# Optimization experiments

Measured on AMD Instinct MI355X. Metric: run time of the kernel, lower is better.

## Reference

```python
import jax, jax.numpy as jnp
import numpy as np

B, D, V = 2048, 512, 50304


def setup_inputs() -> dict:
    key = jax.random.key(0)
    ks = jax.random.split(key, 7)
    scale = 1.0 / np.sqrt(D)
    return {
        "student_h": jax.random.normal(ks[0], (B, D), dtype=jnp.float32) * scale,
        "student_c": jax.random.normal(ks[1], (V, D), dtype=jnp.float32) * scale,
        "teacher_h": jax.random.normal(ks[2], (B, D), dtype=jnp.float32) * scale,
        "teacher_c": jax.random.normal(ks[3], (V, D), dtype=jnp.float32) * scale,
        "ce_coeff": jax.random.uniform(ks[4], (B,), dtype=jnp.float32),
        "kl_coeff": jax.random.uniform(ks[5], (B,), dtype=jnp.float32),
        "targets": jax.random.randint(ks[6], (B,), 0, V, dtype=jnp.int64),
    }


def reference(student_h, student_c, teacher_h, teacher_c, ce_coeff, kl_coeff, targets):
    # Fused linear head: student/teacher logits over the full vocab  [B, V]
    s_logits = jnp.einsum("bd,vd->bv", student_h, student_c)
    t_logits = jnp.einsum("bd,vd->bv", teacher_h, teacher_c)

    s_lse = jax.nn.logsumexp(s_logits, axis=1)  # [B]
    t_lse = jax.nn.logsumexp(t_logits, axis=1)  # [B]

    # Cross-entropy per row: lse - logit[target]
    tgt_logit = jnp.take_along_axis(s_logits, targets[:, None], axis=1)[:, 0]
    ce = s_lse - tgt_logit  # [B]

    # KL(teacher || student) per row
    log_ps = s_logits - s_lse[:, None]
    log_pt = t_logits - t_lse[:, None]
    pt = jnp.exp(log_pt)
    kl = jnp.sum(pt * (log_pt - log_ps), axis=1)  # [B]

    # Per-row coefficients absorb any reduction weighting (as in the kernel)
    loss = jnp.sum(ce_coeff * ce + kl_coeff * kl)
    return loss
```

## Files before the change

kernel.cpp:

```cpp
#include <hip/hip_runtime.h>
#include <hip/hip_fp8.h>

#define B_ 2048
#define D_ 512
#define V_ 50304
#define NROWB 16
#define NCOLB 393
#define NWG (NROWB * NCOLB)
#define LOG2E 1.44269504088896340736f
#define LN2 0.69314718055994530942f

typedef __attribute__((ext_vector_type(4))) float f32x4;
typedef __attribute__((ext_vector_type(2))) unsigned long ulx2;
typedef unsigned char u8;

__device__ inline void gload16(const void* g, void* l) {
  __builtin_amdgcn_global_load_lds((const __attribute__((address_space(1))) void*)g,
                                   (__attribute__((address_space(3))) void*)l, 16, 0, 0);
}

__global__ void cast8_kernel(const float* __restrict__ src, uint2* __restrict__ dst,
                             float scale, int n8) {
  int i = blockIdx.x * blockDim.x + threadIdx.x;
  int stride = gridDim.x * blockDim.x;
  const float4* s4 = (const float4*)src;
  for (; i < n8; i += stride) {
    float4 a = s4[2 * i], b = s4[2 * i + 1];
    union { u8 c[8]; uint2 u; } p;
    p.c[0] = __hip_fp8_e4m3(a.x * scale).__x;
    p.c[1] = __hip_fp8_e4m3(a.y * scale).__x;
    p.c[2] = __hip_fp8_e4m3(a.z * scale).__x;
    p.c[3] = __hip_fp8_e4m3(a.w * scale).__x;
    p.c[4] = __hip_fp8_e4m3(b.x * scale).__x;
    p.c[5] = __hip_fp8_e4m3(b.y * scale).__x;
    p.c[6] = __hip_fp8_e4m3(b.z * scale).__x;
    p.c[7] = __hip_fp8_e4m3(b.w * scale).__x;
    dst[i] = p.u;
  }
}

__global__ void tgt_kernel(const float* __restrict__ sh, const float* __restrict__ sc,
                           const int* __restrict__ targets, float* __restrict__ tgt_out) {
  int gid = blockIdx.x * blockDim.x + threadIdx.x;
  int w = gid >> 6, lane = gid & 63;
  if (w >= B_) return;
  int tgt = targets[w];
  const float4* a = (const float4*)(sh + (size_t)w * D_);
  const float4* b = (const float4*)(sc + (size_t)tgt * D_);
  float acc = 0.f;
#pragma unroll
  for (int i = 0; i < 2; ++i) {
    float4 x = a[lane + i * 64], y = b[lane + i * 64];
    acc += x.x * y.x + x.y * y.y + x.z * y.z + x.w * y.w;
  }
#pragma unroll
  for (int off = 1; off < 64; off <<= 1) acc += __shfl_xor(acc, off);
  if (lane == 0) tgt_out[w] = acc;
}

__global__ __launch_bounds__(256, 2) void lce_main(
    const u8* __restrict__ SH8, const u8* __restrict__ TH8,
    const u8* __restrict__ SC8, const u8* __restrict__ TC8,
    float* __restrict__ stats) {
  __shared__ __align__(16) u8 smem[2][2][128][128];

  const int tid = threadIdx.x;
  const int lane = tid & 63, w = tid >> 6;
  const int mat = w & 1;
  const int wr = w >> 1;
  const int rA = lane & 15;
  const int kg = lane >> 4;
  const int r7 = rA & 7;

  int hw = blockIdx.x;
  int lid = (hw & 7) * 786 + (hw >> 3);
  const int row0 = (lid & 15) * 128;
  const int col0 = (lid >> 4) * 128;

  const int srow_lo = (lane >> 3);
  const int sq = ((lane & 7) ^ srow_lo) * 16;
  const u8* gB[2] = {SC8 + (size_t)(col0 + w * 32 + srow_lo) * D_ + sq,
                     TC8 + (size_t)(col0 + w * 32 + srow_lo) * D_ + sq};

  const u8* gA = (mat ? TH8 : SH8) + (size_t)(row0 + wr * 64 + rA) * D_ + kg * 16;

  f32x4 acc[4][8];
#pragma unroll
  for (int i = 0; i < 4; ++i)
#pragma unroll
    for (int j = 0; j < 8; ++j) acc[i][j] = (f32x4){0.f, 0.f, 0.f, 0.f};

  ulx2 afr[2][2][4];

#define STAGE(buf, kk)                                                        \
  {                                                                           \
    _Pragma("unroll") for (int t = 0; t < 2; ++t) {                           \
      _Pragma("unroll") for (int i = 0; i < 4; ++i) {                         \
        gload16(gB[t] + (size_t)(i * 8) * D_ + (kk) * 128,                    \
                &smem[buf][t][w * 32 + i * 8][0]);                            \
      }                                                                       \
    }                                                                         \
  }

#define LOADA(par, kk)                                                        \
  {                                                                           \
    _Pragma("unroll") for (int mi = 0; mi < 4; ++mi) {                        \
      const u8* p = gA + (size_t)(mi * 16) * D_ + (kk) * 128;                 \
      afr[par][0][mi] = *(const ulx2*)p;                                      \
      afr[par][1][mi] = *(const ulx2*)(p + 64);                               \
    }                                                                         \
  }

  STAGE(0, 0);
  LOADA(0, 0);

#pragma unroll
  for (int kk = 0; kk < 4; ++kk) {
    const int par = kk & 1;
    if (kk < 3) {
      STAGE(par ^ 1, kk + 1);
      LOADA(par ^ 1, kk + 1);
    }
    if (kk < 3)
      asm volatile("s_waitcnt vmcnt(16)\n\ts_barrier" ::: "memory");
    else
      asm volatile("s_waitcnt vmcnt(8)\n\ts_barrier" ::: "memory");

#pragma unroll
    for (int hp = 0; hp < 2; ++hp) {
      ulx2 bfr[8];
#pragma unroll
      for (int ni = 0; ni < 8; ++ni)
        bfr[ni] = *(const ulx2*)&smem[par][mat][ni * 16 + rA][((hp * 4 + kg) ^ r7) * 16];
      __builtin_amdgcn_s_setprio(1);
#pragma unroll
      for (int mi = 0; mi < 4; ++mi)
#pragma unroll
        for (int ni = 0; ni < 8; ++ni) {
          acc[mi][ni] = __builtin_amdgcn_mfma_f32_16x16x32_fp8_fp8(
              (long)afr[par][hp][mi].x, (long)bfr[ni].x, acc[mi][ni], 0, 0, 0);
          acc[mi][ni] = __builtin_amdgcn_mfma_f32_16x16x32_fp8_fp8(
              (long)afr[par][hp][mi].y, (long)bfr[ni].y, acc[mi][ni], 0, 0, 0);
        }
      __builtin_amdgcn_s_setprio(0);
    }
    asm volatile("s_barrier" ::: "memory");
  }

  const float inv = 1.0f / 256.0f;
  float2* exch = (float2*)smem;

  if (mat == 0) {
#pragma unroll
    for (int mi = 0; mi < 4; ++mi)
#pragma unroll
      for (int ni = 0; ni < 8; ++ni)
#pragma unroll
        for (int rp = 0; rp < 2; ++rp) {
          float2 v = make_float2(acc[mi][ni][2 * rp] * inv, acc[mi][ni][2 * rp + 1] * inv);
          exch[(size_t)((((wr * 4 + mi) * 8 + ni) * 2 + rp) * 64 + lane)] = v;
        }
  }
  asm volatile("s_waitcnt lgkmcnt(0)\n\ts_barrier" ::: "memory");

  if (mat == 0) {
#pragma unroll
    for (int mi = 0; mi < 4; ++mi) {
      float ssr[4] = {0.f, 0.f, 0.f, 0.f};
#pragma unroll
      for (int ni = 0; ni < 8; ++ni)
#pragma unroll
        for (int reg = 0; reg < 4; ++reg)
          ssr[reg] += __builtin_amdgcn_exp2f(acc[mi][ni][reg] * inv);
#pragma unroll
      for (int reg = 0; reg < 4; ++reg) {
        float v = ssr[reg];
#pragma unroll
        for (int off = 1; off < 16; off <<= 1) v += __shfl_xor(v, off);
        if (rA == 0)
          atomicAdd(&stats[(size_t)(row0 + wr * 64 + mi * 16 + kg * 4 + reg) * 3 + 0], v);
      }
    }
  } else {
#pragma unroll
    for (int mi = 0; mi < 4; ++mi) {
      float str[4] = {0.f, 0.f, 0.f, 0.f};
      float atr[4] = {0.f, 0.f, 0.f, 0.f};
#pragma unroll
      for (int ni = 0; ni < 8; ++ni)
#pragma unroll
        for (int rp = 0; rp < 2; ++rp) {
          float2 sv = exch[(size_t)((((wr * 4 + mi) * 8 + ni) * 2 + rp) * 64 + lane)];
          float tv0 = acc[mi][ni][2 * rp] * inv;
          float tv1 = acc[mi][ni][2 * rp + 1] * inv;
          float et0 = __builtin_amdgcn_exp2f(tv0);
          float et1 = __builtin_amdgcn_exp2f(tv1);
          str[2 * rp] += et0;
          str[2 * rp + 1] += et1;
          atr[2 * rp] += et0 * (tv0 - sv.x);
          atr[2 * rp + 1] += et1 * (tv1 - sv.y);
        }
#pragma unroll
      for (int reg = 0; reg < 4; ++reg) {
        float v = str[reg], u = atr[reg];
#pragma unroll
        for (int off = 1; off < 16; off <<= 1) {
          v += __shfl_xor(v, off);
          u += __shfl_xor(u, off);
        }
        if (rA == 0) {
          size_t r = (size_t)(row0 + wr * 64 + mi * 16 + kg * 4 + reg) * 3;
          atomicAdd(&stats[r + 1], v);
          atomicAdd(&stats[r + 2], u);
        }
      }
    }
  }
}

__global__ void finalize(const float* __restrict__ stats, const float* __restrict__ tgt,
                         const float* __restrict__ cec, const float* __restrict__ klc,
                         float* __restrict__ out) {
  __shared__ float red[16];
  int tid = threadIdx.x;
  float acc = 0.f;
  for (int r = tid; r < B_; r += 1024) {
    float ss = stats[r * 3 + 0], st = stats[r * 3 + 1], at = stats[r * 3 + 2];
    float s_lse = LN2 * __builtin_amdgcn_logf(ss);
    float t_lse = LN2 * __builtin_amdgcn_logf(st);
    float kl = s_lse - t_lse + LN2 * at / st;
    float ce = s_lse - tgt[r];
    acc += cec[r] * ce + klc[r] * kl;
  }
#pragma unroll
  for (int off = 1; off < 64; off <<= 1) acc += __shfl_xor(acc, off);
  if ((tid & 63) == 0) red[tid >> 6] = acc;
  __syncthreads();
  if (tid == 0) {
    float s = 0.f;
#pragma unroll
    for (int i = 0; i < 16; ++i) s += red[i];
    out[0] = s;
  }
}

extern "C" void kernel_launch(void* const* d_in, const int* in_sizes, int n_in,
                              void* d_out, int out_size, void* d_ws, size_t ws_size,
                              hipStream_t stream) {
  const float* sh = (const float*)d_in[0];
  const float* sc = (const float*)d_in[1];
  const float* th = (const float*)d_in[2];
  const float* tc = (const float*)d_in[3];
  const float* cec = (const float*)d_in[4];
  const float* klc = (const float*)d_in[5];
  const int* targets = (const int*)d_in[6];
  float* out = (float*)d_out;

  char* ws = (char*)d_ws;
  u8* SC8 = (u8*)ws;
  u8* TC8 = SC8 + (size_t)V_ * D_;
  u8* SH8 = TC8 + (size_t)V_ * D_;
  u8* TH8 = SH8 + (size_t)B_ * D_;
  float* stats = (float*)(TH8 + (size_t)B_ * D_);
  float* tgt = stats + (size_t)B_ * 3;

  hipMemsetAsync(stats, 0, (size_t)B_ * 3 * sizeof(float), stream);
  const float hscale = 16.0f * LOG2E;
  const float cscale = 16.0f;
  cast8_kernel<<<2048, 256, 0, stream>>>(sc, (uint2*)SC8, cscale, V_ * D_ / 8);
  cast8_kernel<<<2048, 256, 0, stream>>>(tc, (uint2*)TC8, cscale, V_ * D_ / 8);
  cast8_kernel<<<256, 256, 0, stream>>>(sh, (uint2*)SH8, hscale, B_ * D_ / 8);
  cast8_kernel<<<256, 256, 0, stream>>>(th, (uint2*)TH8, hscale, B_ * D_ / 8);
  tgt_kernel<<<512, 256, 0, stream>>>(sh, sc, targets, tgt);

  lce_main<<<NWG, 256, 0, stream>>>(SH8, TH8, SC8, TC8, stats);
  finalize<<<1, 1024, 0, stream>>>(stats, tgt, cec, klc, out);
}
```

Baseline: 268.9 us.

## Use 16x16x128 scaled FP8 MFMA with pre-tiled classifier layout

Replaces the pairs of 16x16x32 fp8 MFMAs with the gfx950 scaled 16x16x128 f8f6f4 MFMA (unit scales), cutting instruction count per K step by four. To feed the wider B operand cheaply, the classifier matrices are cast into a tile-blocked layout so that LDS staging is fully contiguous per thread and the old XOR swizzle is dropped. The A fragments become 32-byte loads per lane. This risks LDS bank conflicts in the new layout, and a mismatch between the operand K ordering and the layouts would give wrong results.

```diff
diff --git a/kernel.cpp b/kernel.cpp
--- a/kernel.cpp
+++ b/kernel.cpp
@@ -12,11 +12,33 @@
 
 typedef __attribute__((ext_vector_type(4))) float f32x4;
 typedef __attribute__((ext_vector_type(2))) unsigned long ulx2;
+typedef __attribute__((ext_vector_type(8))) int v8i;
 typedef unsigned char u8;
 
 __device__ inline void gload16(const void* g, void* l) {
   __builtin_amdgcn_global_load_lds((const __attribute__((address_space(1))) void*)g,
                                    (__attribute__((address_space(3))) void*)l, 16, 0, 0);
+}
+
+__global__ void cast8t_kernel(const float* __restrict__ src, uint4* __restrict__ dst,
+                              float scale, int nchunk) {
+  int i = blockIdx.x * blockDim.x + threadIdx.x;
+  if (i >= nchunk) return;
+  int c = i & 127;
+  int j = (i >> 7) & 7;
+  int kk = (i >> 10) & 3;
+  int p = i >> 12;
+  const float4* s = (const float4*)(src + (size_t)(p * 128 + c) * 512 + kk * 128 + j * 16);
+  union { u8 b[16]; uint4 u; } o;
+#pragma unroll
+  for (int q = 0; q < 4; ++q) {
+    float4 f = s[q];
+    o.b[q * 4 + 0] = __hip_fp8_e4m3(f.x * scale).__x;
+    o.b[q * 4 + 1] = __hip_fp8_e4m3(f.y * scale).__x;
+    o.b[q * 4 + 2] = __hip_fp8_e4m3(f.z * scale).__x;
+    o.b[q * 4 + 3] = __hip_fp8_e4m3(f.w * scale).__x;
+  }
+  dst[i] = o.u;
 }
 
 __global__ void cast8_kernel(const float* __restrict__ src, uint2* __restrict__ dst,
@@ -60,9 +82,9 @@
 
 __global__ __launch_bounds__(256, 2) void lce_main(
     const u8* __restrict__ SH8, const u8* __restrict__ TH8,
-    const u8* __restrict__ SC8, const u8* __restrict__ TC8,
+    const u8* __restrict__ SC8t, const u8* __restrict__ TC8t,
     float* __restrict__ stats) {
-  __shared__ __align__(16) u8 smem[2][2][128][128];
+  __shared__ __align__(16) u8 smem[2][2][16384];
 
   const int tid = threadIdx.x;
   const int lane = tid & 63, w = tid >> 6;
@@ -70,19 +92,17 @@
   const int wr = w >> 1;
   const int rA = lane & 15;
   const int kg = lane >> 4;
-  const int r7 = rA & 7;
 
   int hw = blockIdx.x;
   int lid = (hw & 7) * 786 + (hw >> 3);
   const int row0 = (lid & 15) * 128;
-  const int col0 = (lid >> 4) * 128;
-
-  const int srow_lo = (lane >> 3);
-  const int sq = ((lane & 7) ^ srow_lo) * 16;
-  const u8* gB[2] = {SC8 + (size_t)(col0 + w * 32 + srow_lo) * D_ + sq,
-                     TC8 + (size_t)(col0 + w * 32 + srow_lo) * D_ + sq};
-
-  const u8* gA = (mat ? TH8 : SH8) + (size_t)(row0 + wr * 64 + rA) * D_ + kg * 16;
+  const int p = lid >> 4;
+  const int col0 = p * 128;
+
+  const u8* gB[2] = {SC8t + (size_t)p * 65536 + tid * 16,
+                     TC8t + (size_t)p * 65536 + tid * 16};
+
+  const u8* gA = (mat ? TH8 : SH8) + (size_t)(row0 + wr * 64 + rA) * D_ + kg * 32;
 
   f32x4 acc[4][8];
 #pragma unroll
@@ -90,24 +110,22 @@
 #pragma unroll
     for (int j = 0; j < 8; ++j) acc[i][j] = (f32x4){0.f, 0.f, 0.f, 0.f};
 
-  ulx2 afr[2][2][4];
+  v8i av[2][4];
 
 #define STAGE(buf, kk)                                                        \
   {                                                                           \
-    _Pragma("unroll") for (int t = 0; t < 2; ++t) {                           \
-      _Pragma("unroll") for (int i = 0; i < 4; ++i) {                         \
-        gload16(gB[t] + (size_t)(i * 8) * D_ + (kk) * 128,                    \
-                &smem[buf][t][w * 32 + i * 8][0]);                            \
+    _Pragma("unroll") for (int mt = 0; mt < 2; ++mt) {                        \
+      _Pragma("unroll") for (int r = 0; r < 4; ++r) {                         \
+        gload16(gB[mt] + (kk) * 16384 + r * 4096,                             \
+                &smem[buf][mt][r * 4096 + tid * 16]);                         \
       }                                                                       \
     }                                                                         \
   }
 
-#define LOADA(par, kk)                                                        \
+#define LOADA(buf, kk)                                                        \
   {                                                                           \
     _Pragma("unroll") for (int mi = 0; mi < 4; ++mi) {                        \
-      const u8* p = gA + (size_t)(mi * 16) * D_ + (kk) * 128;                 \
-      afr[par][0][mi] = *(const ulx2*)p;                                      \
-      afr[par][1][mi] = *(const ulx2*)(p + 64);                               \
+      av[buf][mi] = *(const v8i*)(gA + (size_t)(mi * 16) * D_ + (kk) * 128);  \
     }                                                                         \
   }
 
@@ -126,24 +144,19 @@
     else
       asm volatile("s_waitcnt vmcnt(8)\n\ts_barrier" ::: "memory");
 
-#pragma unroll
-    for (int hp = 0; hp < 2; ++hp) {
-      ulx2 bfr[8];
-#pragma unroll
-      for (int ni = 0; ni < 8; ++ni)
-        bfr[ni] = *(const ulx2*)&smem[par][mat][ni * 16 + rA][((hp * 4 + kg) ^ r7) * 16];
-      __builtin_amdgcn_s_setprio(1);
+    __builtin_amdgcn_s_setprio(1);
+#pragma unroll
+    for (int ni = 0; ni < 8; ++ni) {
+      const u8* bp = &smem[par][mat][(2 * kg) * 2048 + (ni * 16 + rA) * 16];
+      union { struct { ulx2 lo, hi; } s; v8i v; } ub;
+      ub.s.lo = *(const ulx2*)bp;
+      ub.s.hi = *(const ulx2*)(bp + 2048);
 #pragma unroll
       for (int mi = 0; mi < 4; ++mi)
-#pragma unroll
-        for (int ni = 0; ni < 8; ++ni) {
-          acc[mi][ni] = __builtin_amdgcn_mfma_f32_16x16x32_fp8_fp8(
-              (long)afr[par][hp][mi].x, (long)bfr[ni].x, acc[mi][ni], 0, 0, 0);
-          acc[mi][ni] = __builtin_amdgcn_mfma_f32_16x16x32_fp8_fp8(
-              (long)afr[par][hp][mi].y, (long)bfr[ni].y, acc[mi][ni], 0, 0, 0);
-        }
-      __builtin_amdgcn_s_setprio(0);
-    }
+        acc[mi][ni] = __builtin_amdgcn_mfma_scale_f32_16x16x128_f8f6f4(
+            av[par][mi], ub.v, acc[mi][ni], 0, 0, 0, 127, 0, 127);
+    }
+    __builtin_amdgcn_s_setprio(0);
     asm volatile("s_barrier" ::: "memory");
   }
 
@@ -257,9 +270,9 @@
   float* out = (float*)d_out;
 
   char* ws = (char*)d_ws;
-  u8* SC8 = (u8*)ws;
-  u8* TC8 = SC8 + (size_t)V_ * D_;
-  u8* SH8 = TC8 + (size_t)V_ * D_;
+  u8* SC8t = (u8*)ws;
+  u8* TC8t = SC8t + (size_t)V_ * D_;
+  u8* SH8 = TC8t + (size_t)V_ * D_;
   u8* TH8 = SH8 + (size_t)B_ * D_;
   float* stats = (float*)(TH8 + (size_t)B_ * D_);
   float* tgt = stats + (size_t)B_ * 3;
@@ -267,12 +280,13 @@
   hipMemsetAsync(stats, 0, (size_t)B_ * 3 * sizeof(float), stream);
   const float hscale = 16.0f * LOG2E;
   const float cscale = 16.0f;
-  cast8_kernel<<<2048, 256, 0, stream>>>(sc, (uint2*)SC8, cscale, V_ * D_ / 8);
-  cast8_kernel<<<2048, 256, 0, stream>>>(tc, (uint2*)TC8, cscale, V_ * D_ / 8);
+  const int nchunk = V_ * D_ / 16;
+  cast8t_kernel<<<(nchunk + 255) / 256, 256, 0, stream>>>(sc, (uint4*)SC8t, cscale, nchunk);
+  cast8t_kernel<<<(nchunk + 255) / 256, 256, 0, stream>>>(tc, (uint4*)TC8t, cscale, nchunk);
   cast8_kernel<<<256, 256, 0, stream>>>(sh, (uint2*)SH8, hscale, B_ * D_ / 8);
   cast8_kernel<<<256, 256, 0, stream>>>(th, (uint2*)TH8, hscale, B_ * D_ / 8);
   tgt_kernel<<<512, 256, 0, stream>>>(sh, sc, targets, tgt);
 
-  lce_main<<<NWG, 256, 0, stream>>>(SH8, TH8, SC8, TC8, stats);
+  lce_main<<<NWG, 256, 0, stream>>>(SH8, TH8, SC8t, TC8t, stats);
   finalize<<<1, 1024, 0, stream>>>(stats, tgt, cec, klc, out);
 }
```

Result: slower. 328.3 us (+22.1%).
